# Kernel optimization log

Measured on AMD Instinct MI355X. Metric: run time of the kernel, lower is better.

## Reference

```python
import jax, jax.numpy as jnp
import numpy as np

NEG_SLOPE = 0.2


def setup_inputs() -> dict:
    key = jax.random.key(0)
    k1, k2, k3 = jax.random.split(key, 3)
    B, C, F_in, F_out = 8, 2048, 64, 64
    node_features = jax.random.normal(k1, (B, C, F_in), dtype=jnp.float32)
    # nn.Linear weight: [out_features, in_features]
    W = jax.random.normal(k2, (F_out, F_in), dtype=jnp.float32) * (1.0 / np.sqrt(F_in))
    # attention vector a: [2*F_out, 1], xavier-uniform style init
    bound = float(np.sqrt(6.0 / (2 * F_out + 1)))
    a = jax.random.uniform(k3, (2 * F_out, 1), dtype=jnp.float32, minval=-bound, maxval=bound)
    return {"node_features": node_features, "W": W, "a": a}


def reference(node_features, W, a):
    # Wh: [B, C, F_out]
    Wh = jnp.einsum("bcf,of->bco", node_features, W)
    F_out = W.shape[0]
    a1 = a[:F_out, 0]  # scores for the i (row) side
    a2 = a[F_out:, 0]  # scores for the j (col) side
    # Decompose concat([Wh_i, Wh_j]) @ a == Wh_i@a1 + Wh_j@a2 (avoids [B,C,C,2F] tensor)
    s1 = Wh @ a1  # [B, C]
    s2 = Wh @ a2  # [B, C]
    e = jax.nn.leaky_relu(s1[:, :, None] + s2[:, None, :], negative_slope=NEG_SLOPE)  # [B,C,C]
    attention = jax.nn.softmax(e, axis=-1)
    out = jnp.einsum("bij,bjo->bio", attention, Wh)  # weighted aggregate
    return jax.nn.elu(out), attention
```

## Files before the change

### kernel.cpp

```cpp
#include <hip/hip_runtime.h>

typedef float f32x4 __attribute__((ext_vector_type(4)));
typedef _Float16 half8 __attribute__((ext_vector_type(8)));

#define NEG 0.2f

__global__ __launch_bounds__(256) void gat_wh_kernel(
    const float* __restrict__ nf, const float* __restrict__ W,
    const float* __restrict__ a, _Float16* __restrict__ whT,
    float* __restrict__ s1g, float* __restrict__ s2g, float* __restrict__ smax)
{
    const int b    = blockIdx.x >> 5;
    const int rb   = blockIdx.x & 31;
    const int row0 = rb * 64;
    const int t    = threadIdx.x;
    const int lane = t & 63;
    const int wv   = t >> 6;

    __shared__ _Float16 whL[64][72];
    __shared__ float    wred[4];

    f32x4 Wreg[16];
    const float* wp = W + lane * 64;
#pragma unroll
    for (int i = 0; i < 16; ++i) Wreg[i] = *(const f32x4*)(wp + i * 4);
    const float a1v = a[lane];
    const float a2v = a[64 + lane];

    const float* nfb = nf + ((long)b * 2048 + row0) * 64;
    float wmax = -3.0e38f;

    for (int g = 0; g < 16; ++g) {
        const int row = g * 4 + wv;
        const f32x4* nfp = (const f32x4*)(nfb + row * 64);
        f32x4 acc = {0.f, 0.f, 0.f, 0.f};
#pragma unroll
        for (int i = 0; i < 16; ++i) acc += nfp[i] * Wreg[i];
        const float wh = acc.x + acc.y + acc.z + acc.w;
        whL[row][lane] = (_Float16)wh;
        float p1 = wh * a1v;
        float p2 = wh * a2v;
#pragma unroll
        for (int m = 32; m >= 1; m >>= 1) {
            p1 += __shfl_xor(p1, m);
            p2 += __shfl_xor(p2, m);
        }
        if (lane == 0) {
            s1g[b * 2048 + row0 + row] = p1;
            s2g[b * 2048 + row0 + row] = p2;
            wmax = fmaxf(wmax, p2);
        }
    }
    if (lane == 0) wred[wv] = wmax;
    __syncthreads();
    if (t == 0)
        smax[blockIdx.x] = fmaxf(fmaxf(wred[0], wred[1]), fmaxf(wred[2], wred[3]));

    const int o = t >> 2;
    const int part = t & 3;
    unsigned int tmp[8];
#pragma unroll
    for (int kk = 0; kk < 8; ++kk) {
        const int j = part * 16 + kk * 2;
        unsigned int lo = *(const unsigned short*)&whL[j][o];
        unsigned int hi = *(const unsigned short*)&whL[j + 1][o];
        tmp[kk] = lo | (hi << 16);
    }
    uint4 v0, v1;
    v0.x = tmp[0]; v0.y = tmp[1]; v0.z = tmp[2]; v0.w = tmp[3];
    v1.x = tmp[4]; v1.y = tmp[5]; v1.z = tmp[6]; v1.w = tmp[7];
    _Float16* dst = whT + ((long)(b * 64 + o) * 2048 + row0 + part * 16);
    *(uint4*)dst = v0;
    *(uint4*)(dst + 8) = v1;
}

__global__ __launch_bounds__(256) void gat_attn_kernel(
    const _Float16* __restrict__ whT, const float* __restrict__ s1g,
    const float* __restrict__ s2g, const float* __restrict__ smax,
    float* __restrict__ outp)
{
    const int b    = blockIdx.x >> 7;
    const int rb   = blockIdx.x & 127;
    const int i0   = rb * 16;
    const int t    = threadIdx.x;
    const int lane = t & 63;
    const int wv   = t >> 6;

    __shared__ __attribute__((aligned(16))) float s2sh[2048];
    __shared__ float s1sh[16], Msh[16], iDsh[16];
    __shared__ float m2sh;
    __shared__ __attribute__((aligned(16))) _Float16 Pl[2][16][72];

#pragma unroll
    for (int k = 0; k < 8; ++k) s2sh[t + k * 256] = s2g[b * 2048 + t + k * 256];
    if (t < 16) s1sh[t] = s1g[b * 2048 + i0 + t];
    if (t < 32) {
        float v = smax[b * 32 + t];
#pragma unroll
        for (int m = 16; m >= 1; m >>= 1) v = fmaxf(v, __shfl_xor(v, m));
        if (t == 0) m2sh = v;
    }
    __syncthreads();

    {
        const float m2  = m2sh;
        const int   r   = t >> 4, q = t & 15;
        const float s1r = s1sh[r];
        const float xm  = s1r + m2;
        const float M   = fmaxf(xm, NEG * xm);
        float acc = 0.f;
        for (int j = q; j < 2048; j += 16) {
            float x = s1r + s2sh[j];
            float e = fmaxf(x, NEG * x);
            acc += __expf(e - M);
        }
        acc += __shfl_xor(acc, 1);
        acc += __shfl_xor(acc, 2);
        acc += __shfl_xor(acc, 4);
        acc += __shfl_xor(acc, 8);
        if (q == 0) { Msh[r] = M; iDsh[r] = 1.0f / acc; }
    }
    __syncthreads();

    float s1v[4], Mv[4], iDv[4];
#pragma unroll
    for (int k = 0; k < 4; ++k) {
        s1v[k] = s1sh[wv * 4 + k];
        Mv[k]  = Msh[wv * 4 + k];
        iDv[k] = iDsh[wv * 4 + k];
    }

    f32x4 acc0 = {0.f, 0.f, 0.f, 0.f};
    const int koff = (lane >> 4) * 8;
    const _Float16* Bp = whT + (long)b * 64 * 2048
                       + (long)(wv * 16 + (lane & 15)) * 2048 + koff;
    float* attnb = outp + 1048576 + ((long)b * 2048 + i0 + wv * 4) * 2048;

    for (int c = 0; c < 32; ++c) {
        const int j0  = c * 64;
        const int buf = c & 1;

        half8 b0 = *(const half8*)(Bp + j0);
        half8 b1 = *(const half8*)(Bp + j0 + 32);

        const float sv = s2sh[j0 + lane];
#pragma unroll
        for (int k = 0; k < 4; ++k) {
            float x = s1v[k] + sv;
            float e = fmaxf(x, NEG * x);
            float p = __expf(e - Mv[k]) * iDv[k];
            attnb[(long)k * 2048 + j0 + lane] = p;
            Pl[buf][wv * 4 + k][lane] = (_Float16)p;
        }
        __syncthreads();

        half8 a0 = *(const half8*)&Pl[buf][lane & 15][koff];
        half8 a1 = *(const half8*)&Pl[buf][lane & 15][koff + 32];
        acc0 = __builtin_amdgcn_mfma_f32_16x16x32_f16(a0, b0, acc0, 0, 0, 0);
        acc0 = __builtin_amdgcn_mfma_f32_16x16x32_f16(a1, b1, acc0, 0, 0, 0);
    }

    {
        const int col = wv * 16 + (lane & 15);
        float* ob = outp + ((long)b * 2048 + i0 + (lane >> 4) * 4) * 64 + col;
#pragma unroll
        for (int r = 0; r < 4; ++r) {
            float x = acc0[r];
            ob[(long)r * 64] = (x > 0.f) ? x : (__expf(x) - 1.0f);
        }
    }
}

extern "C" void kernel_launch(void* const* d_in, const int* in_sizes, int n_in,
                              void* d_out, int out_size, void* d_ws, size_t ws_size,
                              hipStream_t stream)
{
    (void)in_sizes; (void)n_in; (void)out_size; (void)ws_size;
    const float* nf = (const float*)d_in[0];
    const float* W  = (const float*)d_in[1];
    const float* a  = (const float*)d_in[2];
    float* outp = (float*)d_out;

    char* ws = (char*)d_ws;
    _Float16* whT = (_Float16*)ws;
    float* s1g  = (float*)(ws + 2097152);
    float* s2g  = (float*)(ws + 2097152 + 65536);
    float* smax = (float*)(ws + 2097152 + 131072);

    gat_wh_kernel<<<256, 256, 0, stream>>>(nf, W, a, whT, s1g, s2g, smax);
    gat_attn_kernel<<<1024, 256, 0, stream>>>(whT, s1g, s2g, smax, outp);
}
```

Measured before the change: 72.62 us.

## Split softmax denominator into its own kernel and decouple attention store from MFMA

After: 84.03 us. 15.7% more time.

```diff
diff --git a/kernel.cpp b/kernel.cpp
--- a/kernel.cpp
+++ b/kernel.cpp
@@ -74,99 +74,138 @@
     *(uint4*)(dst + 8) = v1;
 }
 
-__global__ __launch_bounds__(256) void gat_attn_kernel(
+__global__ __launch_bounds__(256) void gat_denom_kernel(
+    const float* __restrict__ s1g, const float* __restrict__ s2g,
+    const float* __restrict__ smax, float* __restrict__ m2g,
+    float* __restrict__ iDg)
+{
+    const int b  = blockIdx.x >> 6;
+    const int i0 = (blockIdx.x & 63) * 32;
+    const int t  = threadIdx.x;
+
+    __shared__ __attribute__((aligned(16))) float s2sh[2048];
+    __shared__ float m2sh;
+
+#pragma unroll
+    for (int k = 0; k < 8; ++k) s2sh[t + k * 256] = s2g[b * 2048 + t + k * 256];
+    if (t < 32) {
+        float v = smax[b * 32 + t];
+#pragma unroll
+        for (int m = 16; m >= 1; m >>= 1) v = fmaxf(v, __shfl_xor(v, m));
+        if (t == 0) m2sh = v;
+    }
+    __syncthreads();
+
+    const float m2  = m2sh;
+    const int   r   = t >> 3, q = t & 7;
+    const float s1r = s1g[b * 2048 + i0 + r];
+    const float xm  = s1r + m2;
+    const float M   = fmaxf(xm, NEG * xm);
+    float acc = 0.f;
+    for (int j = q; j < 2048; j += 8) {
+        float x = s1r + s2sh[j];
+        float e = fmaxf(x, NEG * x);
+        acc += __expf(e - M);
+    }
+    acc += __shfl_xor(acc, 1);
+    acc += __shfl_xor(acc, 2);
+    acc += __shfl_xor(acc, 4);
+    if (q == 0) iDg[b * 2048 + i0 + r] = 1.0f / acc;
+    if ((blockIdx.x & 63) == 0 && t == 0) m2g[b] = m2;
+}
+
+__global__ __launch_bounds__(256) void gat_main_kernel(
     const _Float16* __restrict__ whT, const float* __restrict__ s1g,
-    const float* __restrict__ s2g, const float* __restrict__ smax,
-    float* __restrict__ outp)
-{
-    const int b    = blockIdx.x >> 7;
-    const int rb   = blockIdx.x & 127;
-    const int i0   = rb * 16;
+    const float* __restrict__ s2g, const float* __restrict__ m2g,
+    const float* __restrict__ iDg, float* __restrict__ outp)
+{
     const int t    = threadIdx.x;
     const int lane = t & 63;
     const int wv   = t >> 6;
 
-    __shared__ __attribute__((aligned(16))) float s2sh[2048];
-    __shared__ float s1sh[16], Msh[16], iDsh[16];
-    __shared__ float m2sh;
-    __shared__ __attribute__((aligned(16))) _Float16 Pl[2][16][72];
-
-#pragma unroll
-    for (int k = 0; k < 8; ++k) s2sh[t + k * 256] = s2g[b * 2048 + t + k * 256];
-    if (t < 16) s1sh[t] = s1g[b * 2048 + i0 + t];
-    if (t < 32) {
-        float v = smax[b * 32 + t];
-#pragma unroll
-        for (int m = 16; m >= 1; m >>= 1) v = fmaxf(v, __shfl_xor(v, m));
-        if (t == 0) m2sh = v;
-    }
-    __syncthreads();
-
-    {
-        const float m2  = m2sh;
-        const int   r   = t >> 4, q = t & 15;
-        const float s1r = s1sh[r];
+    if (blockIdx.x < 256) {
+        const int b  = blockIdx.x >> 5;
+        const int i0 = (blockIdx.x & 31) * 64 + wv * 16;
+        const int q  = lane & 15;
+        const int g  = lane >> 4;
+        const int row = i0 + q;
+
+        const float s1r = s1g[b * 2048 + row];
+        const float m2  = m2g[b];
         const float xm  = s1r + m2;
-        const float M   = fmaxf(xm, NEG * xm);
-        float acc = 0.f;
-        for (int j = q; j < 2048; j += 16) {
-            float x = s1r + s2sh[j];
-            float e = fmaxf(x, NEG * x);
-            acc += __expf(e - M);
-        }
-        acc += __shfl_xor(acc, 1);
-        acc += __shfl_xor(acc, 2);
-        acc += __shfl_xor(acc, 4);
-        acc += __shfl_xor(acc, 8);
-        if (q == 0) { Msh[r] = M; iDsh[r] = 1.0f / acc; }
-    }
-    __syncthreads();
-
-    float s1v[4], Mv[4], iDv[4];
-#pragma unroll
-    for (int k = 0; k < 4; ++k) {
-        s1v[k] = s1sh[wv * 4 + k];
-        Mv[k]  = Msh[wv * 4 + k];
-        iDv[k] = iDsh[wv * 4 + k];
-    }
-
-    f32x4 acc0 = {0.f, 0.f, 0.f, 0.f};
-    const int koff = (lane >> 4) * 8;
-    const _Float16* Bp = whT + (long)b * 64 * 2048
-                       + (long)(wv * 16 + (lane & 15)) * 2048 + koff;
-    float* attnb = outp + 1048576 + ((long)b * 2048 + i0 + wv * 4) * 2048;
-
-    for (int c = 0; c < 32; ++c) {
-        const int j0  = c * 64;
-        const int buf = c & 1;
-
-        half8 b0 = *(const half8*)(Bp + j0);
-        half8 b1 = *(const half8*)(Bp + j0 + 32);
-
-        const float sv = s2sh[j0 + lane];
-#pragma unroll
-        for (int k = 0; k < 4; ++k) {
-            float x = s1v[k] + sv;
-            float e = fmaxf(x, NEG * x);
-            float p = __expf(e - Mv[k]) * iDv[k];
-            attnb[(long)k * 2048 + j0 + lane] = p;
-            Pl[buf][wv * 4 + k][lane] = (_Float16)p;
-        }
-        __syncthreads();
-
-        half8 a0 = *(const half8*)&Pl[buf][lane & 15][koff];
-        half8 a1 = *(const half8*)&Pl[buf][lane & 15][koff + 32];
-        acc0 = __builtin_amdgcn_mfma_f32_16x16x32_f16(a0, b0, acc0, 0, 0, 0);
-        acc0 = __builtin_amdgcn_mfma_f32_16x16x32_f16(a1, b1, acc0, 0, 0, 0);
-    }
-
-    {
-        const int col = wv * 16 + (lane & 15);
-        float* ob = outp + ((long)b * 2048 + i0 + (lane >> 4) * 4) * 64 + col;
+        const float Mr  = fmaxf(xm, NEG * xm);
+        const float iDr = iDg[b * 2048 + row];
+
+        const float*    s2p = s2g + b * 2048 + g * 8;
+        const _Float16* B0  = whT + ((long)(b * 64 + q)) * 2048 + g * 8;
+
+        f32x4 acc0 = {0.f,0.f,0.f,0.f}, acc1 = {0.f,0.f,0.f,0.f};
+        f32x4 acc2 = {0.f,0.f,0.f,0.f}, acc3 = {0.f,0.f,0.f,0.f};
+
+        for (int kk = 0; kk < 64; ++kk) {
+            const int j0 = kk * 32;
+            half8 b0 = *(const half8*)(B0 + j0);
+            half8 b1 = *(const half8*)(B0 + 16 * 2048 + j0);
+            half8 b2 = *(const half8*)(B0 + 32 * 2048 + j0);
+            half8 b3 = *(const half8*)(B0 + 48 * 2048 + j0);
+
+            f32x4 sa = *(const f32x4*)(s2p + j0);
+            f32x4 sb = *(const f32x4*)(s2p + j0 + 4);
+            half8 a;
+#pragma unroll
+            for (int e = 0; e < 4; ++e) {
+                float x  = s1r + sa[e];
+                float lr = fmaxf(x, NEG * x);
+                a[e] = (_Float16)(__expf(lr - Mr) * iDr);
+                float y  = s1r + sb[e];
+                float lq = fmaxf(y, NEG * y);
+                a[e + 4] = (_Float16)(__expf(lq - Mr) * iDr);
+            }
+            acc0 = __builtin_amdgcn_mfma_f32_16x16x32_f16(a, b0, acc0, 0, 0, 0);
+            acc1 = __builtin_amdgcn_mfma_f32_16x16x32_f16(a, b1, acc1, 0, 0, 0);
+            acc2 = __builtin_amdgcn_mfma_f32_16x16x32_f16(a, b2, acc2, 0, 0, 0);
+            acc3 = __builtin_amdgcn_mfma_f32_16x16x32_f16(a, b3, acc3, 0, 0, 0);
+        }
+
+        float* ob = outp + ((long)(b * 2048 + i0 + g * 4)) * 64 + q;
 #pragma unroll
         for (int r = 0; r < 4; ++r) {
-            float x = acc0[r];
-            ob[(long)r * 64] = (x > 0.f) ? x : (__expf(x) - 1.0f);
+            float x0 = acc0[r], x1 = acc1[r], x2 = acc2[r], x3 = acc3[r];
+            ob[(long)r * 64]      = (x0 > 0.f) ? x0 : (__expf(x0) - 1.0f);
+            ob[(long)r * 64 + 16] = (x1 > 0.f) ? x1 : (__expf(x1) - 1.0f);
+            ob[(long)r * 64 + 32] = (x2 > 0.f) ? x2 : (__expf(x2) - 1.0f);
+            ob[(long)r * 64 + 48] = (x3 > 0.f) ? x3 : (__expf(x3) - 1.0f);
+        }
+    } else {
+        const int sb = blockIdx.x - 256;
+        const int b  = sb >> 8;
+        const int r0 = (sb & 255) * 8 + wv * 2;
+
+        const float* s2b = s2g + b * 2048;
+        const float  m2  = m2g[b];
+        float* attnb = outp + 1048576 + ((long)b * 2048 + r0) * 2048;
+
+#pragma unroll
+        for (int rr = 0; rr < 2; ++rr) {
+            const int row  = r0 + rr;
+            const float s1r = s1g[b * 2048 + row];
+            const float xm  = s1r + m2;
+            const float Mr  = fmaxf(xm, NEG * xm);
+            const float iDr = iDg[b * 2048 + row];
+            float* arow = attnb + (long)rr * 2048;
+#pragma unroll
+            for (int cc = 0; cc < 8; ++cc) {
+                const int j = cc * 256 + lane * 4;
+                f32x4 s = *(const f32x4*)(s2b + j);
+                f32x4 p;
+#pragma unroll
+                for (int e = 0; e < 4; ++e) {
+                    float x  = s1r + s[e];
+                    float lr = fmaxf(x, NEG * x);
+                    p[e] = __expf(lr - Mr) * iDr;
+                }
+                __builtin_nontemporal_store(p, (f32x4*)(arow + j));
+            }
         }
     }
 }
@@ -184,9 +223,12 @@
     char* ws = (char*)d_ws;
     _Float16* whT = (_Float16*)ws;
     float* s1g  = (float*)(ws + 2097152);
-    float* s2g  = (float*)(ws + 2097152 + 65536);
-    float* smax = (float*)(ws + 2097152 + 131072);
+    float* s2g  = (float*)(ws + 2162688);
+    float* smax = (float*)(ws + 2228224);
+    float* m2g  = (float*)(ws + 2229248);
+    float* iDg  = (float*)(ws + 2230272);
 
     gat_wh_kernel<<<256, 256, 0, stream>>>(nf, W, a, whT, s1g, s2g, smax);
-    gat_attn_kernel<<<1024, 256, 0, stream>>>(whT, s1g, s2g, smax, outp);
-}
+    gat_denom_kernel<<<512, 256, 0, stream>>>(s1g, s2g, smax, m2g, iDg);
+    gat_main_kernel<<<2304, 256, 0, stream>>>(whT, s1g, s2g, m2g, iDg, outp);
+}
```
